# Kernel tuning notes

Measured on AMD Instinct MI355X. Metric: run time of the kernel, lower is better.

The kernel has to match this reference:

```python
import jax, jax.numpy as jnp
import numpy as np
import heapq

V = 10000   # vocab size (number of Huffman leaves)
H = 768     # hidden_size
B = 8       # batch
S = 256     # sen_len


def _build_tree():
    """Replicates make_heap/merge_nodes/make_codes: returns padded path tables.
    path_nodes[v, d] = internal-node index (0..V-2) at step d on v's code path,
    path_bits[v, d]  = branch taken (0=left, 1=right), path_mask = valid steps.
    """
    rng = np.random.default_rng(0)
    freqs = rng.integers(1, 1000, size=V)
    heap = [(int(freqs[i]), i, i) for i in range(V)]  # (freq, tiebreak, node_id)
    heapq.heapify(heap)
    left, right = {}, {}
    nid = V
    uid = V
    while len(heap) > 1:
        fa, _, a = heapq.heappop(heap)
        fb, _, b = heapq.heappop(heap)
        left[nid] = a
        right[nid] = b
        heapq.heappush(heap, (fa + fb, uid, nid))
        nid += 1
        uid += 1
    root = heap[0][2]
    paths = [None] * V
    stack = [(root, [], [])]
    while stack:
        n, pn, pb = stack.pop()
        if n < V:
            paths[n] = (pn, pb)
        else:
            idx = n - V  # internal node index into node_W/node_b
            stack.append((left[n], pn + [idx], pb + [0]))
            stack.append((right[n], pn + [idx], pb + [1]))
    D = max(len(p[0]) for p in paths)
    pn = np.zeros((V, D), np.int32)
    pb = np.zeros((V, D), np.int32)
    pm = np.zeros((V, D), bool)
    for i, (ns, bs) in enumerate(paths):
        L = len(ns)
        pn[i, :L] = ns
        pb[i, :L] = bs
        pm[i, :L] = True
    return pn, pb, pm


def setup_inputs() -> dict:
    key = jax.random.key(0)
    k1, k2, k3, k4 = jax.random.split(key, 4)
    pn, pb, pm = _build_tree()
    bound = float(1.0 / np.sqrt(H))  # torch nn.Linear default init
    return {
        "hidden": jax.random.normal(k1, (B, S, H), jnp.float32),
        "target": jax.random.randint(k2, (B, S), 0, V),
        "node_W": jax.random.uniform(k3, (V - 1, H, 2), jnp.float32, -bound, bound),
        "node_b": jax.random.uniform(k4, (V - 1, 2), jnp.float32, -bound, bound),
        "path_nodes": jnp.asarray(pn),
        "path_bits": jnp.asarray(pb),
        "path_mask": jnp.asarray(pm),
    }


def reference(hidden, target, node_W, node_b, path_nodes, path_bits, path_mask):
    # hidden: [B,S,H] -> [T,H]; target: [B,S] -> [T]
    h = hidden.reshape(-1, hidden.shape[-1])
    t = target.reshape(-1)
    nodes = path_nodes[t]          # [T, D] internal-node ids along each token's path
    bits = path_bits[t]            # [T, D] branch targets
    mask = path_mask[t]            # [T, D] valid-step mask
    Wg = node_W[nodes]             # [T, D, H, 2] gathered per-path linear weights
    bg = node_b[nodes]             # [T, D, 2]
    logits = jnp.einsum('th,tdho->tdo', h, Wg) + bg  # [T, D, 2]
    # Faithful to original: CrossEntropyLoss applied to Softmax OUTPUT (double softmax)
    probs = jax.nn.softmax(logits, axis=-1)
    logp = jax.nn.log_softmax(probs, axis=-1)
    ce = -jnp.take_along_axis(logp, bits[..., None], axis=-1)[..., 0]  # [T, D]
    # Original accumulates per-step CE (each over batch of 1) by summation
    return jnp.sum(jnp.where(mask, ce, jnp.zeros_like(ce)))
```

## Files before the change

kernel.cpp:

```cpp
#include <hip/hip_runtime.h>

#define HID 768
#define NTHREADS 256
#define WPB 4
#define RTHREADS 256

__global__ __launch_bounds__(NTHREADS) void huffman_step_kernel(
    const float* __restrict__ hidden,
    const int*   __restrict__ target,
    const float* __restrict__ node_W,
    const float* __restrict__ node_b,
    const int*   __restrict__ path_nodes,
    const int*   __restrict__ path_bits,
    const void*  __restrict__ path_mask,
    float*       __restrict__ partial,
    int D)
{
    const int t    = blockIdx.x;
    const int wave = threadIdx.x >> 6;
    const int lane = threadIdx.x & 63;
    const int d    = blockIdx.y * WPB + wave;
    const int slot = (blockIdx.x * gridDim.y + blockIdx.y) * WPB + wave;

    float result = 0.0f;

    if (d < D) {
        const bool mask_is_byte = (*(const unsigned int*)path_mask) > 1u;

        const int v = target[t];
        const long prow = (long)v * D + d;
        const bool valid = mask_is_byte
            ? (((const unsigned char*)path_mask)[prow] != 0)
            : (((const int*)path_mask)[prow] != 0);

        if (valid) {
            const int n = path_nodes[prow];
            const float4* __restrict__ w4 =
                (const float4*)(node_W + (long)n * (HID * 2));
            const float2* __restrict__ h2 =
                (const float2*)(hidden + (long)t * HID);

            float acc0 = 0.0f, acc1 = 0.0f;
            #pragma unroll
            for (int j = 0; j < HID / 2 / 64; ++j) {
                const int p = j * 64 + lane;
                const float4 w = w4[p];
                const float2 h = h2[p];
                acc0 += h.x * w.x + h.y * w.z;
                acc1 += h.x * w.y + h.y * w.w;
            }

            #pragma unroll
            for (int off = 32; off > 0; off >>= 1) {
                acc0 += __shfl_xor(acc0, off, 64);
                acc1 += __shfl_xor(acc1, off, 64);
            }

            const float l0 = acc0 + node_b[n * 2 + 0];
            const float l1 = acc1 + node_b[n * 2 + 1];
            const float m  = fmaxf(l0, l1);
            const float e0 = __expf(l0 - m);
            const float e1 = __expf(l1 - m);
            const float s  = e0 + e1;
            const float p0 = e0 / s;
            const float p1 = e1 / s;
            const float lse = __logf(__expf(p0) + __expf(p1));
            const float pb  = path_bits[prow] ? p1 : p0;
            result = lse - pb;
        }
    }

    if (lane == 0) partial[slot] = result;
}

__global__ __launch_bounds__(RTHREADS) void huffman_reduce_kernel(
    const float* __restrict__ partial, float* __restrict__ out, int n4)
{
    const float4* __restrict__ p4 = (const float4*)partial;
    float s = 0.0f;
    for (int i = threadIdx.x; i < n4; i += RTHREADS) {
        const float4 v = p4[i];
        s += (v.x + v.y) + (v.z + v.w);
    }
    #pragma unroll
    for (int off = 32; off > 0; off >>= 1) s += __shfl_xor(s, off, 64);
    __shared__ float ws[RTHREADS / 64];
    if ((threadIdx.x & 63) == 0) ws[threadIdx.x >> 6] = s;
    __syncthreads();
    if (threadIdx.x == 0) {
        float tot = 0.0f;
        #pragma unroll
        for (int w = 0; w < RTHREADS / 64; ++w) tot += ws[w];
        out[0] = tot;
    }
}

extern "C" void kernel_launch(void* const* d_in, const int* in_sizes, int n_in,
                              void* d_out, int out_size, void* d_ws, size_t ws_size,
                              hipStream_t stream) {
    const float* hidden     = (const float*)d_in[0];
    const int*   target     = (const int*)d_in[1];
    const float* node_W     = (const float*)d_in[2];
    const float* node_b     = (const float*)d_in[3];
    const int*   path_nodes = (const int*)d_in[4];
    const int*   path_bits  = (const int*)d_in[5];
    const void*  path_mask  = (const void*)d_in[6];
    float* out = (float*)d_out;
    float* partial = (float*)d_ws;

    const int T   = in_sizes[0] / HID;
    const int Vm1 = in_sizes[3] / 2;
    const int V   = Vm1 + 1;
    const int D   = in_sizes[4] / V;

    const int gy    = (D + WPB - 1) / WPB;
    const int nslot = T * gy * WPB;

    huffman_step_kernel<<<dim3(T, gy), dim3(NTHREADS), 0, stream>>>(
        hidden, target, node_W, node_b, path_nodes, path_bits, path_mask,
        partial, D);

    huffman_reduce_kernel<<<dim3(1), dim3(RTHREADS), 0, stream>>>(
        partial, out, nslot / 4);
}
```

Baseline: 130.8 us.

## Process all path steps per token in one block with prefetched weights

Each block now handles one token: four waves stride over the depth dimension, holding the hidden row in registers and prefetching the next node's weights while computing the current one. The grid shrinks from T x ceil(D/4) blocks to T blocks, and waves stop early at the first invalid step instead of launching blocks for padded steps. The partial buffer the reduction sums becomes smaller. The trade-offs are fewer blocks, which means less parallelism for latency hiding, a serial dependency chain per wave, and higher register use.

```diff
diff --git a/kernel.cpp b/kernel.cpp
--- a/kernel.cpp
+++ b/kernel.cpp
@@ -5,7 +5,7 @@
 #define WPB 4
 #define RTHREADS 256
 
-__global__ __launch_bounds__(NTHREADS) void huffman_step_kernel(
+__global__ __launch_bounds__(NTHREADS) void huffman_token_kernel(
     const float* __restrict__ hidden,
     const int*   __restrict__ target,
     const float* __restrict__ node_W,
@@ -19,58 +19,73 @@
     const int t    = blockIdx.x;
     const int wave = threadIdx.x >> 6;
     const int lane = threadIdx.x & 63;
-    const int d    = blockIdx.y * WPB + wave;
-    const int slot = (blockIdx.x * gridDim.y + blockIdx.y) * WPB + wave;
 
-    float result = 0.0f;
+    const bool mask_is_byte = (*(const unsigned int*)path_mask) > 1u;
+    const unsigned char* __restrict__ mb = (const unsigned char*)path_mask;
+    const int*           __restrict__ mi = (const int*)path_mask;
 
-    if (d < D) {
-        const bool mask_is_byte = (*(const unsigned int*)path_mask) > 1u;
+    const int v = target[t];
 
-        const int v = target[t];
-        const long prow = (long)v * D + d;
-        const bool valid = mask_is_byte
-            ? (((const unsigned char*)path_mask)[prow] != 0)
-            : (((const int*)path_mask)[prow] != 0);
+    const float2* __restrict__ h2 = (const float2*)(hidden + (long)t * HID);
+    float2 h[6];
+    #pragma unroll
+    for (int j = 0; j < 6; ++j) h[j] = h2[j * 64 + lane];
 
-        if (valid) {
-            const int n = path_nodes[prow];
-            const float4* __restrict__ w4 =
-                (const float4*)(node_W + (long)n * (HID * 2));
-            const float2* __restrict__ h2 =
-                (const float2*)(hidden + (long)t * HID);
+    float sum = 0.0f;
 
-            float acc0 = 0.0f, acc1 = 0.0f;
-            #pragma unroll
-            for (int j = 0; j < HID / 2 / 64; ++j) {
-                const int p = j * 64 + lane;
-                const float4 w = w4[p];
-                const float2 h = h2[p];
-                acc0 += h.x * w.x + h.y * w.z;
-                acc1 += h.x * w.y + h.y * w.w;
-            }
+    int  d    = wave;
+    long prow = (long)v * D + wave;
 
-            #pragma unroll
-            for (int off = 32; off > 0; off >>= 1) {
-                acc0 += __shfl_xor(acc0, off, 64);
-                acc1 += __shfl_xor(acc1, off, 64);
-            }
+    bool valid = (d < D) && (mask_is_byte ? (mb[prow] != 0) : (mi[prow] != 0));
+    int  n     = valid ? path_nodes[prow] : 0;
 
-            const float l0 = acc0 + node_b[n * 2 + 0];
-            const float l1 = acc1 + node_b[n * 2 + 1];
-            const float m  = fmaxf(l0, l1);
-            const float e0 = __expf(l0 - m);
-            const float e1 = __expf(l1 - m);
-            const float s  = e0 + e1;
-            const float p0 = e0 / s;
-            const float p1 = e1 / s;
-            const float lse = __logf(__expf(p0) + __expf(p1));
-            const float pb  = path_bits[prow] ? p1 : p0;
-            result = lse - pb;
+    const float4* __restrict__ w4 = (const float4*)(node_W + (long)n * (HID * 2));
+    float4 w[6];
+    #pragma unroll
+    for (int j = 0; j < 6; ++j) w[j] = w4[j * 64 + lane];
+
+    while (valid) {
+        const long prow2  = prow + WPB;
+        const int  d2     = d + WPB;
+        const bool valid2 = (d2 < D) &&
+            (mask_is_byte ? (mb[prow2] != 0) : (mi[prow2] != 0));
+        const int  n2     = valid2 ? path_nodes[prow2] : 0;
+        const float4* __restrict__ w4n =
+            (const float4*)(node_W + (long)n2 * (HID * 2));
+        float4 wn[6];
+        #pragma unroll
+        for (int j = 0; j < 6; ++j) wn[j] = w4n[j * 64 + lane];
+
+        float acc0 = 0.0f, acc1 = 0.0f;
+        #pragma unroll
+        for (int j = 0; j < 6; ++j) {
+            acc0 += h[j].x * w[j].x + h[j].y * w[j].z;
+            acc1 += h[j].x * w[j].y + h[j].y * w[j].w;
         }
+        #pragma unroll
+        for (int off = 32; off > 0; off >>= 1) {
+            acc0 += __shfl_xor(acc0, off, 64);
+            acc1 += __shfl_xor(acc1, off, 64);
+        }
+
+        const float l0  = acc0 + node_b[n * 2 + 0];
+        const float l1  = acc1 + node_b[n * 2 + 1];
+        const float m   = fmaxf(l0, l1);
+        const float e0  = __expf(l0 - m);
+        const float e1  = __expf(l1 - m);
+        const float s   = e0 + e1;
+        const float p0  = e0 / s;
+        const float p1  = e1 / s;
+        const float lse = __logf(__expf(p0) + __expf(p1));
+        const float pb  = path_bits[prow] ? p1 : p0;
+        sum += lse - pb;
+
+        prow = prow2; d = d2; n = n2; valid = valid2;
+        #pragma unroll
+        for (int j = 0; j < 6; ++j) w[j] = wn[j];
     }
 
-    if (lane == 0) partial[slot] = result;
+    if (lane == 0) partial[t * WPB + wave] = sum;
 }
 
 __global__ __launch_bounds__(RTHREADS) void huffman_reduce_kernel(
@@ -113,10 +128,9 @@
     const int V   = Vm1 + 1;
     const int D   = in_sizes[4] / V;
 
-    const int gy    = (D + WPB - 1) / WPB;
-    const int nslot = T * gy * WPB;
+    const int nslot = T * WPB;
 
-    huffman_step_kernel<<<dim3(T, gy), dim3(NTHREADS), 0, stream>>>(
+    huffman_token_kernel<<<dim3(T), dim3(NTHREADS), 0, stream>>>(
         hidden, target, node_W, node_b, path_nodes, path_bits, path_mask,
         partial, D);
 
```

Result: faster. 117.7 us (-10.1%).
